# Kernel optimization log

Hardware: AMD Instinct MI355X
Metric: run time of the kernel (lower is better)

## Reference

```python
import jax, jax.numpy as jnp
import numpy as np

NUM_HEADS = 16


def setup_inputs() -> dict:
    key = jax.random.key(0)
    k1, k2, k3 = jax.random.split(key, 3)
    B, S, D = 2, 2048, 1024
    x = jax.random.normal(k1, (B, S, D), dtype=jnp.float32)
    # qkv_bias=False -> no bias on qkv projection; output Dense has default bias
    w_qkv = jax.random.normal(k2, (D, 3 * D), dtype=jnp.float32) * (1.0 / np.sqrt(D))
    w_out = jax.random.normal(k3, (D, D), dtype=jnp.float32) * (1.0 / np.sqrt(D))
    b_out = jnp.zeros((D,), dtype=jnp.float32)
    return {"x": x, "w_qkv": w_qkv, "w_out": w_out, "b_out": b_out}


def reference(x, w_qkv, w_out, b_out):
    B, S, D = x.shape
    H = NUM_HEADS
    Dh = D // H
    scale = 1.0 / np.sqrt(Dh).astype(np.float32)

    qkv = jnp.einsum('bsd,de->bse', x, w_qkv)           # [B,S,3D]
    q, k, v = jnp.split(qkv, 3, axis=-1)
    split = lambda t: t.reshape(B, S, H, Dh).transpose(0, 2, 1, 3)  # [B,H,S,Dh]
    q, k, v = split(q), split(k), split(v)

    attn = jnp.einsum('bhid,bhjd->bhij', q, k) * scale  # [B,H,S,S]
    # mask=None -> all-ones mask combined with causal mask => causal float mask
    causal = jnp.tril(jnp.ones((S, S), dtype=jnp.float32))[None, None]
    attn = causal * attn + (1.0 - causal) * (-1e9)
    attn = jax.nn.softmax(attn, axis=-1)

    out = jnp.einsum('bhij,bhjd->bhid', attn, v)        # [B,H,S,Dh]
    out = out.transpose(0, 2, 1, 3).reshape(B, S, D)    # merge heads
    return jnp.einsum('bsd,de->bse', out, w_out) + b_out
```

## Files before the change

kernel.cpp:

```cpp
#include <hip/hip_runtime.h>

typedef unsigned short u16;
typedef __bf16 bf16x8 __attribute__((ext_vector_type(8)));
typedef unsigned short u16x8 __attribute__((ext_vector_type(8)));
typedef float f32x4 __attribute__((ext_vector_type(4)));

union Frag { u16x8 u; bf16x8 b; };

__device__ __forceinline__ u16 f2bf(float f) {
  unsigned u = __builtin_bit_cast(unsigned, f);
  u += 0x7fff + ((u >> 16) & 1);
  return (u16)(u >> 16);
}

__device__ __forceinline__ f32x4 mfma16(bf16x8 a, bf16x8 b, f32x4 c) {
  return __builtin_amdgcn_mfma_f32_16x16x32_bf16(a, b, c, 0, 0, 0);
}

__device__ __forceinline__ float exp2_raw(float x) {
  float r;
  asm("v_exp_f32 %0, %1" : "=v"(r) : "v"(x));
  return r;
}

typedef const __attribute__((address_space(1))) void* as1cv;
typedef __attribute__((address_space(3))) void* as3v;

__device__ __forceinline__ void glds16(const u16* g, u16* l) {
  __builtin_amdgcn_global_load_lds((as1cv)g, (as3v)l, 16, 0, 0);
}

__global__ __launch_bounds__(256) void prep(const float* __restrict__ x,
                                            u16* __restrict__ xb,
                                            const float* __restrict__ wqkv,
                                            u16* __restrict__ wqkvT,
                                            const float* __restrict__ wout,
                                            u16* __restrict__ woutT) {
  __shared__ float tile[32][33];
  int bid = blockIdx.x;
  int tid = threadIdx.x;
  if (bid >= 4096) {
    int i = (bid - 4096) * 256 + tid;
    const int stride = 1024 * 256;
#pragma unroll
    for (int k = 0; k < 4; ++k) {
      float4 v = ((const float4*)x)[i];
      ushort4 o;
      o.x = f2bf(v.x); o.y = f2bf(v.y); o.z = f2bf(v.z); o.w = f2bf(v.w);
      ((ushort4*)xb)[i] = o;
      i += stride;
    }
    return;
  }
  const float* src; u16* dst; int N;
  if (bid < 3072) { src = wqkv; dst = wqkvT; N = 3072; }
  else            { bid -= 3072; src = wout; dst = woutT; N = 1024; }
  const int K = 1024;
  int tn = N >> 5;
  int bk = bid / tn, bn = bid % tn;
  int k0 = bk << 5, n0 = bn << 5;
  int tx = tid & 31, ty = tid >> 5;
#pragma unroll
  for (int i = 0; i < 4; i++)
    tile[ty + 8 * i][tx] = src[(size_t)(k0 + ty + 8 * i) * N + n0 + tx];
  __syncthreads();
#pragma unroll
  for (int i = 0; i < 4; i++)
    dst[(size_t)(n0 + ty + 8 * i) * K + k0 + tx] = f2bf(tile[tx][ty + 8 * i]);
}

__global__ __launch_bounds__(256) void gemm_qkv(const u16* __restrict__ A,
                                                const u16* __restrict__ BT,
                                                u16* __restrict__ C,
                                                u16* __restrict__ vt,
                                                int N, int K, int nbc) {
  __shared__ u16 Al[2][128 * 32];
  __shared__ u16 Bl[2][128 * 32];
  int nwg = gridDim.x;
  int bid = blockIdx.x;
  int swz = (bid & 7) * (nwg >> 3) + (bid >> 3);
  int br = swz / nbc, bc = swz % nbc;
  int tid = threadIdx.x;
  int w = tid >> 6, l = tid & 63;
  int lg = l >> 4, lq = l & 15;
  int wr = w >> 1, wc = w & 1;

  f32x4 acc[4][4];
#pragma unroll
  for (int m = 0; m < 4; m++)
#pragma unroll
    for (int n = 0; n < 4; n++)
      acc[m][n] = (f32x4){0.f, 0.f, 0.f, 0.f};

  const u16* Ab = A + (size_t)(br * 128 + 32 * w + (l >> 2)) * K + (l & 3) * 8;
  const u16* Bb = BT + (size_t)(bc * 128 + 32 * w + (l >> 2)) * K + (l & 3) * 8;

  auto stage = [&](int it, int buf) {
    int kt = it * 32;
    u16* ald = &Al[buf][32 * w * 32];
    u16* bld = &Bl[buf][32 * w * 32];
    glds16(Ab + kt, ald);
    glds16(Ab + (size_t)16 * K + kt, ald + 16 * 32);
    glds16(Bb + kt, bld);
    glds16(Bb + (size_t)16 * K + kt, bld + 16 * 32);
  };

  int nk = K >> 5;
  stage(0, 0);
  __syncthreads();

  for (int it = 0; it < nk; ++it) {
    int buf = it & 1;
    if (it + 1 < nk) stage(it + 1, buf ^ 1);

    Frag af[4], bf[4];
#pragma unroll
    for (int m = 0; m < 4; m++)
      af[m].u = *(const u16x8*)(&Al[buf][(64 * wr + 16 * m + lq) * 32 + lg * 8]);
#pragma unroll
    for (int n = 0; n < 4; n++)
      bf[n].u = *(const u16x8*)(&Bl[buf][(64 * wc + 16 * n + lq) * 32 + lg * 8]);
    __builtin_amdgcn_s_setprio(1);
#pragma unroll
    for (int m = 0; m < 4; m++)
#pragma unroll
      for (int n = 0; n < 4; n++)
        acc[m][n] = mfma16(af[m].b, bf[n].b, acc[m][n]);
    __builtin_amdgcn_s_setprio(0);
    __syncthreads();
  }

  int row0 = br * 128 + 64 * wr + lg * 4;
  int col0 = bc * 128 + 64 * wc + lq;
  if (bc < 16) {
#pragma unroll
    for (int n = 0; n < 4; n++)
#pragma unroll
      for (int m = 0; m < 4; m++)
#pragma unroll
        for (int r = 0; r < 4; r++)
          C[(size_t)(row0 + 16 * m + r) * N + col0 + 16 * n] = f2bf(acc[m][n][r]);
  } else {
    u16* stbuf = (w == 0) ? &Al[0][0] : (w == 1) ? &Al[1][0]
               : (w == 2) ? &Bl[0][0] : &Bl[1][0];
#pragma unroll
    for (int m = 0; m < 4; m++)
#pragma unroll
      for (int r = 0; r < 4; r++) {
        int srow = 16 * m + 4 * lg + r;
        int X = ((srow >> 2) & 7) << 3;
#pragma unroll
        for (int n = 0; n < 4; n++)
          stbuf[srow * 64 + ((16 * n + lq) ^ X)] = f2bf(acc[m][n][r]);
      }
    int a = l >> 3, bgrp = l & 7;
    int s_base = br * 128 + 64 * wr;
    int bb = s_base >> 11;
    int sblk = (s_base & 2047) >> 6;
    int hh = ((bc - 16) << 1) | wc;
    size_t vbase = ((size_t)(bb * 16 + hh) * 32 + sblk) * 4096;
#pragma unroll
    for (int j = 0; j < 8; ++j) {
      int dh = 8 * j + a;
      u16x8 v;
#pragma unroll
      for (int i = 0; i < 8; ++i) {
        int srow = ((bgrp >> 2) << 5) | (((i >> 2) & 1) << 4) |
                   ((bgrp & 3) << 2) | (i & 3);
        int X = ((srow >> 2) & 7) << 3;
        v[i] = stbuf[srow * 64 + (dh ^ X)];
      }
      *(u16x8*)&vt[vbase + dh * 64 + bgrp * 8] = v;
    }
  }
}

__global__ __launch_bounds__(256) void gemm_bt(const u16* __restrict__ A,
                                               const u16* __restrict__ BT,
                                               float* __restrict__ Cout,
                                               const float* __restrict__ bias,
                                               int N, int K, int nbc) {
  __shared__ u16 Al[2][128 * 32];
  __shared__ u16 Bl[2][128 * 32];
  int nwg = gridDim.x;
  int bid = blockIdx.x;
  int swz = (bid & 7) * (nwg >> 3) + (bid >> 3);
  int br = swz / nbc, bc = swz % nbc;
  int tid = threadIdx.x;
  int w = tid >> 6, l = tid & 63;
  int lg = l >> 4, lq = l & 15;
  int wr = w >> 1, wc = w & 1;

  f32x4 acc[4][4];
#pragma unroll
  for (int m = 0; m < 4; m++)
#pragma unroll
    for (int n = 0; n < 4; n++)
      acc[m][n] = (f32x4){0.f, 0.f, 0.f, 0.f};

  const u16* Ab = A + (size_t)(br * 128 + 32 * w + (l >> 2)) * K + (l & 3) * 8;
  const u16* Bb = BT + (size_t)(bc * 128 + 32 * w + (l >> 2)) * K + (l & 3) * 8;

  auto stage = [&](int it, int buf) {
    int kt = it * 32;
    u16* ald = &Al[buf][32 * w * 32];
    u16* bld = &Bl[buf][32 * w * 32];
    glds16(Ab + kt, ald);
    glds16(Ab + (size_t)16 * K + kt, ald + 16 * 32);
    glds16(Bb + kt, bld);
    glds16(Bb + (size_t)16 * K + kt, bld + 16 * 32);
  };

  int nk = K >> 5;
  stage(0, 0);
  __syncthreads();

  for (int it = 0; it < nk; ++it) {
    int buf = it & 1;
    if (it + 1 < nk) stage(it + 1, buf ^ 1);

    Frag af[4], bf[4];
#pragma unroll
    for (int m = 0; m < 4; m++)
      af[m].u = *(const u16x8*)(&Al[buf][(64 * wr + 16 * m + lq) * 32 + lg * 8]);
#pragma unroll
    for (int n = 0; n < 4; n++)
      bf[n].u = *(const u16x8*)(&Bl[buf][(64 * wc + 16 * n + lq) * 32 + lg * 8]);
    __builtin_amdgcn_s_setprio(1);
#pragma unroll
    for (int m = 0; m < 4; m++)
#pragma unroll
      for (int n = 0; n < 4; n++)
        acc[m][n] = mfma16(af[m].b, bf[n].b, acc[m][n]);
    __builtin_amdgcn_s_setprio(0);
    __syncthreads();
  }

  int row0 = br * 128 + 64 * wr + lg * 4;
  int col0 = bc * 128 + 64 * wc + lq;
#pragma unroll
  for (int n = 0; n < 4; n++) {
    float bv = bias[col0 + 16 * n];
#pragma unroll
    for (int m = 0; m < 4; m++)
#pragma unroll
      for (int r = 0; r < 4; r++)
        Cout[(size_t)(row0 + 16 * m + r) * N + col0 + 16 * n] = acc[m][n][r] + bv;
  }
}

__global__ __launch_bounds__(256) void flash_attn(const u16* __restrict__ qkv,
                                                  const u16* __restrict__ vt,
                                                  u16* __restrict__ aout) {
  __shared__ __align__(16) u16 pool[2][8192];
  const float SL2E = 0.18033688011112043f;
  int bid = blockIdx.x;
  int bh = bid & 31;
  int g = bid >> 5;
  int qb = (g < 8) ? (31 - g) : (g < 16) ? (g - 8) : (g < 24) ? (39 - g) : (g - 16);
  int b = bh >> 4, h = bh & 15;
  int tid = threadIdx.x;
  int w = tid >> 6, l = tid & 63;
  int lg = l >> 4, lq = l & 15;
  int q0w = qb * 64 + w * 16;
  int qidx = q0w + lq;

  const size_t rs = 3072;
  int srw = l >> 3;
  int scol = 8 * ((l & 7) ^ srw);
  const u16* kg = qkv + (size_t)(b * 2048) * rs + 1024 + h * 64;
  const u16* vg = vt + (size_t)bh * 32 * 4096;
  int r0 = (w * 2 + 0) * 8 + srw;
  int r1 = (w * 2 + 1) * 8 + srw;
  int swz = (lq & 7) << 3;

  Frag qf0, qf1;
  const u16* qbase = qkv + (size_t)(b * 2048 + q0w + lq) * rs + h * 64 + lg * 8;
  qf0.u = *(const u16x8*)(qbase);
  qf1.u = *(const u16x8*)(qbase + 32);

  f32x4 lam4 = {0.f, 0.f, 0.f, 0.f};
  f32x4 o[4];
#pragma unroll
  for (int d = 0; d < 4; ++d) o[d] = (f32x4){0.f, 0.f, 0.f, 0.f};

  auto stage = [&](int tile, int buf) {
    int kt2 = tile * 64;
    u16* nb = &pool[buf][0];
    glds16(kg + (size_t)(kt2 + r0) * rs + scol, nb + (w * 2 + 0) * 512);
    glds16(kg + (size_t)(kt2 + r1) * rs + scol, nb + (w * 2 + 1) * 512);
    glds16(vg + (size_t)kt2 * 64 + r0 * 64 + scol, nb + 4096 + (w * 2 + 0) * 512);
    glds16(vg + (size_t)kt2 * 64 + r1 * 64 + scol, nb + 4096 + (w * 2 + 1) * 512);
  };

  stage(0, 0);
  __syncthreads();

  for (int t = 0; t < qb; ++t) {
    stage(t + 1, (t + 1) & 1);
    const u16* Kl = &pool[t & 1][0];
    const u16* Vl = &pool[t & 1][4096];

    f32x4 s[4];
    __builtin_amdgcn_s_setprio(1);
#pragma unroll
    for (int sub = 0; sub < 4; ++sub) {
      int row = sub * 16 + lq;
      Frag k0, k1;
      k0.u = *(const u16x8*)(Kl + row * 64 + ((lg * 8) ^ swz));
      k1.u = *(const u16x8*)(Kl + row * 64 + ((32 + lg * 8) ^ swz));
      f32x4 z = {0.f, 0.f, 0.f, 0.f};
      s[sub] = mfma16(k0.b, qf0.b, z);
      s[sub] = mfma16(k1.b, qf1.b, s[sub]);
    }
    __builtin_amdgcn_s_setprio(0);

    Frag vf[4][2];
#pragma unroll
    for (int d = 0; d < 4; ++d) {
      int row = d * 16 + lq;
      vf[d][0].u = *(const u16x8*)(Vl + row * 64 + ((lg * 8) ^ swz));
      vf[d][1].u = *(const u16x8*)(Vl + row * 64 + ((32 + lg * 8) ^ swz));
    }

    Frag pf[2];
#pragma unroll
    for (int hf = 0; hf < 2; ++hf)
#pragma unroll
      for (int r = 0; r < 4; ++r) {
        float p0 = exp2_raw(s[2 * hf][r] * SL2E);
        float p1 = exp2_raw(s[2 * hf + 1][r] * SL2E);
        lam4[r] += p0 + p1;
        pf[hf].b[r] = (__bf16)p0;
        pf[hf].b[4 + r] = (__bf16)p1;
      }

    __builtin_amdgcn_s_setprio(1);
#pragma unroll
    for (int d = 0; d < 4; ++d) {
      o[d] = mfma16(vf[d][0].b, pf[0].b, o[d]);
      o[d] = mfma16(vf[d][1].b, pf[1].b, o[d]);
    }
    __builtin_amdgcn_s_setprio(0);
    __syncthreads();
  }

  {
    const u16* Kl = &pool[qb & 1][0];
    const u16* Vl = &pool[qb & 1][4096];
    int kt = qb * 64;

    f32x4 s[4];
    __builtin_amdgcn_s_setprio(1);
#pragma unroll
    for (int sub = 0; sub < 4; ++sub) {
      int row = sub * 16 + lq;
      Frag k0, k1;
      k0.u = *(const u16x8*)(Kl + row * 64 + ((lg * 8) ^ swz));
      k1.u = *(const u16x8*)(Kl + row * 64 + ((32 + lg * 8) ^ swz));
      f32x4 z = {0.f, 0.f, 0.f, 0.f};
      s[sub] = mfma16(k0.b, qf0.b, z);
      s[sub] = mfma16(k1.b, qf1.b, s[sub]);
    }
    __builtin_amdgcn_s_setprio(0);

    Frag vf[4][2];
#pragma unroll
    for (int d = 0; d < 4; ++d) {
      int row = d * 16 + lq;
      vf[d][0].u = *(const u16x8*)(Vl + row * 64 + ((lg * 8) ^ swz));
      vf[d][1].u = *(const u16x8*)(Vl + row * 64 + ((32 + lg * 8) ^ swz));
    }

#pragma unroll
    for (int sub = 0; sub < 4; ++sub)
#pragma unroll
      for (int r = 0; r < 4; ++r) {
        int key = kt + sub * 16 + lg * 4 + r;
        if (key > qidx) s[sub][r] = -1e30f;
      }

    Frag pf[2];
#pragma unroll
    for (int hf = 0; hf < 2; ++hf)
#pragma unroll
      for (int r = 0; r < 4; ++r) {
        float p0 = exp2_raw(s[2 * hf][r] * SL2E);
        float p1 = exp2_raw(s[2 * hf + 1][r] * SL2E);
        lam4[r] += p0 + p1;
        pf[hf].b[r] = (__bf16)p0;
        pf[hf].b[4 + r] = (__bf16)p1;
      }

    __builtin_amdgcn_s_setprio(1);
#pragma unroll
    for (int d = 0; d < 4; ++d) {
      o[d] = mfma16(vf[d][0].b, pf[0].b, o[d]);
      o[d] = mfma16(vf[d][1].b, pf[1].b, o[d]);
    }
    __builtin_amdgcn_s_setprio(0);
    __syncthreads();
  }

  float lam = lam4[0] + lam4[1] + lam4[2] + lam4[3];
  lam += __shfl_xor(lam, 16);
  lam += __shfl_xor(lam, 32);
  float inv = 1.0f / lam;

  u16* Ost = &pool[0][0] + w * (16 * 72);
#pragma unroll
  for (int d = 0; d < 4; ++d)
#pragma unroll
    for (int r = 0; r < 4; ++r)
      Ost[lq * 72 + d * 16 + lg * 4 + r] = f2bf(o[d][r] * inv);
  int q = l >> 2, c16 = (l & 3) * 16;
  u16x8 t0, t1;
#pragma unroll
  for (int j = 0; j < 8; j++) { t0[j] = Ost[q * 72 + c16 + j]; t1[j] = Ost[q * 72 + c16 + 8 + j]; }
  u16* orow = aout + (size_t)(b * 2048 + qb * 64 + w * 16 + q) * 1024 + h * 64 + c16;
  *(u16x8*)orow = t0;
  *(u16x8*)(orow + 8) = t1;
}

extern "C" void kernel_launch(void* const* d_in, const int* in_sizes, int n_in,
                              void* d_out, int out_size, void* d_ws, size_t ws_size,
                              hipStream_t stream) {
  const float* x    = (const float*)d_in[0];
  const float* wqkv = (const float*)d_in[1];
  const float* wout = (const float*)d_in[2];
  const float* bout = (const float*)d_in[3];
  float* out = (float*)d_out;

  char* ws = (char*)d_ws;
  u16* xb    = (u16*)(ws);
  u16* wqkvT = (u16*)(ws + 8388608);
  u16* woutT = (u16*)(ws + 14680064);
  u16* qkvb  = (u16*)(ws + 16777216);
  u16* vtb   = (u16*)(ws + 41943040);
  u16* aoutb = (u16*)(ws + 50331648);

  prep<<<5120, 256, 0, stream>>>(x, xb, wqkv, wqkvT, wout, woutT);

  gemm_qkv<<<(4096 / 128) * (3072 / 128), 256, 0, stream>>>(xb, wqkvT, qkvb, vtb,
                                                            3072, 1024, 3072 / 128);
  flash_attn<<<1024, 256, 0, stream>>>(qkvb, vtb, aoutb);

  gemm_bt<<<(4096 / 128) * (1024 / 128), 256, 0, stream>>>(aoutb, woutT, out, bout,
                                                           1024, 1024, 1024 / 128);
}
```

Baseline: 102.2 us.

## Enlarge QKV GEMM tile to 256x256 with 8 waves and triple-buffered LDS

The QKV projection GEMM now uses 256x256 output tiles per workgroup with 512 threads, each wave computing a 128x64 sub-tile. LDS staging moves from double to triple buffering with explicit vmcnt waits and raw barriers, so loads run two stages ahead. This raises operand reuse per LDS byte and hides global latency better. In exchange, register pressure rises (32 accumulators per lane), LDS use grows, and only 192 workgroups are launched, which may underfill the CUs.

```diff
diff --git a/kernel.cpp b/kernel.cpp
--- a/kernel.cpp
+++ b/kernel.cpp
@@ -29,6 +29,8 @@
 __device__ __forceinline__ void glds16(const u16* g, u16* l) {
   __builtin_amdgcn_global_load_lds((as1cv)g, (as3v)l, 16, 0, 0);
 }
+
+#define FENCE asm volatile("" ::: "memory")
 
 __global__ __launch_bounds__(256) void prep(const float* __restrict__ x,
                                             u16* __restrict__ xb,
@@ -69,13 +71,13 @@
     dst[(size_t)(n0 + ty + 8 * i) * K + k0 + tx] = f2bf(tile[tx][ty + 8 * i]);
 }
 
-__global__ __launch_bounds__(256) void gemm_qkv(const u16* __restrict__ A,
+__global__ __launch_bounds__(512) void gemm_qkv(const u16* __restrict__ A,
                                                 const u16* __restrict__ BT,
                                                 u16* __restrict__ C,
                                                 u16* __restrict__ vt,
                                                 int N, int K, int nbc) {
-  __shared__ u16 Al[2][128 * 32];
-  __shared__ u16 Bl[2][128 * 32];
+  __shared__ u16 Al[3][8192];
+  __shared__ u16 Bl[3][8192];
   int nwg = gridDim.x;
   int bid = blockIdx.x;
   int swz = (bid & 7) * (nwg >> 3) + (bid >> 3);
@@ -83,94 +85,103 @@
   int tid = threadIdx.x;
   int w = tid >> 6, l = tid & 63;
   int lg = l >> 4, lq = l & 15;
-  int wr = w >> 1, wc = w & 1;
-
-  f32x4 acc[4][4];
-#pragma unroll
-  for (int m = 0; m < 4; m++)
+  int wr = w >> 2, wc = w & 3;
+
+  f32x4 acc[8][4];
+#pragma unroll
+  for (int m = 0; m < 8; m++)
 #pragma unroll
     for (int n = 0; n < 4; n++)
       acc[m][n] = (f32x4){0.f, 0.f, 0.f, 0.f};
 
-  const u16* Ab = A + (size_t)(br * 128 + 32 * w + (l >> 2)) * K + (l & 3) * 8;
-  const u16* Bb = BT + (size_t)(bc * 128 + 32 * w + (l >> 2)) * K + (l & 3) * 8;
+  const u16* Ab = A + (size_t)(br * 256 + w * 16 + (l >> 2)) * K + (l & 3) * 8;
+  const u16* Bb = BT + (size_t)(bc * 256 + w * 16 + (l >> 2)) * K + (l & 3) * 8;
 
   auto stage = [&](int it, int buf) {
     int kt = it * 32;
-    u16* ald = &Al[buf][32 * w * 32];
-    u16* bld = &Bl[buf][32 * w * 32];
-    glds16(Ab + kt, ald);
-    glds16(Ab + (size_t)16 * K + kt, ald + 16 * 32);
-    glds16(Bb + kt, bld);
-    glds16(Bb + (size_t)16 * K + kt, bld + 16 * 32);
+    glds16(Ab + kt, &Al[buf][w * 512]);
+    glds16(Ab + (size_t)128 * K + kt, &Al[buf][4096 + w * 512]);
+    glds16(Bb + kt, &Bl[buf][w * 512]);
+    glds16(Bb + (size_t)128 * K + kt, &Bl[buf][4096 + w * 512]);
   };
 
   int nk = K >> 5;
   stage(0, 0);
-  __syncthreads();
-
+  stage(1, 1);
+  asm volatile("s_waitcnt vmcnt(4)" ::: "memory");
+  FENCE; __builtin_amdgcn_s_barrier(); FENCE;
+
+  int cur = 0;
   for (int it = 0; it < nk; ++it) {
-    int buf = it & 1;
-    if (it + 1 < nk) stage(it + 1, buf ^ 1);
-
-    Frag af[4], bf[4];
-#pragma unroll
-    for (int m = 0; m < 4; m++)
-      af[m].u = *(const u16x8*)(&Al[buf][(64 * wr + 16 * m + lq) * 32 + lg * 8]);
+    int b2 = cur + 2; if (b2 >= 3) b2 -= 3;
+    if (it + 2 < nk) stage(it + 2, b2);
+
+    Frag a[8], bb[4];
+#pragma unroll
+    for (int m = 0; m < 8; m++)
+      a[m].u = *(const u16x8*)(&Al[cur][(wr * 128 + m * 16 + lq) * 32 + lg * 8]);
 #pragma unroll
     for (int n = 0; n < 4; n++)
-      bf[n].u = *(const u16x8*)(&Bl[buf][(64 * wc + 16 * n + lq) * 32 + lg * 8]);
-    __builtin_amdgcn_s_setprio(1);
-#pragma unroll
-    for (int m = 0; m < 4; m++)
+      bb[n].u = *(const u16x8*)(&Bl[cur][(wc * 64 + n * 16 + lq) * 32 + lg * 8]);
+    __builtin_amdgcn_s_setprio(1);
+#pragma unroll
+    for (int m = 0; m < 8; m++)
 #pragma unroll
       for (int n = 0; n < 4; n++)
-        acc[m][n] = mfma16(af[m].b, bf[n].b, acc[m][n]);
-    __builtin_amdgcn_s_setprio(0);
+        acc[m][n] = mfma16(a[m].b, bb[n].b, acc[m][n]);
+    __builtin_amdgcn_s_setprio(0);
+
+    if (it + 2 < nk)      asm volatile("s_waitcnt vmcnt(4)" ::: "memory");
+    else if (it + 1 < nk) asm volatile("s_waitcnt vmcnt(0)" ::: "memory");
+    if (it + 1 < nk) { FENCE; __builtin_amdgcn_s_barrier(); FENCE; }
+    cur += 1; if (cur >= 3) cur -= 3;
+  }
+
+  int col0 = bc * 256 + wc * 64 + lq;
+  if (bc < 8) {
+#pragma unroll
+    for (int m = 0; m < 8; m++) {
+      int row0 = br * 256 + wr * 128 + m * 16 + lg * 4;
+#pragma unroll
+      for (int n = 0; n < 4; n++)
+#pragma unroll
+        for (int r = 0; r < 4; r++)
+          C[(size_t)(row0 + r) * N + col0 + 16 * n] = f2bf(acc[m][n][r]);
+    }
+  } else {
     __syncthreads();
-  }
-
-  int row0 = br * 128 + 64 * wr + lg * 4;
-  int col0 = bc * 128 + 64 * wc + lq;
-  if (bc < 16) {
-#pragma unroll
-    for (int n = 0; n < 4; n++)
-#pragma unroll
-      for (int m = 0; m < 4; m++)
-#pragma unroll
-        for (int r = 0; r < 4; r++)
-          C[(size_t)(row0 + 16 * m + r) * N + col0 + 16 * n] = f2bf(acc[m][n][r]);
-  } else {
-    u16* stbuf = (w == 0) ? &Al[0][0] : (w == 1) ? &Al[1][0]
-               : (w == 2) ? &Bl[0][0] : &Bl[1][0];
-#pragma unroll
-    for (int m = 0; m < 4; m++)
-#pragma unroll
-      for (int r = 0; r < 4; r++) {
-        int srow = 16 * m + 4 * lg + r;
-        int X = ((srow >> 2) & 7) << 3;
-#pragma unroll
-        for (int n = 0; n < 4; n++)
-          stbuf[srow * 64 + ((16 * n + lq) ^ X)] = f2bf(acc[m][n][r]);
+    u16* stbuf = &Al[0][0] + w * 4096;
+    int hh = (bc - 8) * 4 + wc;
+    int a_ = l >> 3, bgrp = l & 7;
+#pragma unroll
+    for (int sb = 0; sb < 2; ++sb) {
+#pragma unroll
+      for (int mm = 0; mm < 4; mm++)
+#pragma unroll
+        for (int r = 0; r < 4; r++) {
+          int srow = 16 * mm + 4 * lg + r;
+          int X = ((srow >> 2) & 7) << 3;
+#pragma unroll
+          for (int n = 0; n < 4; n++)
+            stbuf[srow * 64 + ((16 * n + lq) ^ X)] = f2bf(acc[sb * 4 + mm][n][r]);
+        }
+      int s_abs = br * 256 + wr * 128 + sb * 64;
+      int bb_ = s_abs >> 11;
+      int sblk = (s_abs & 2047) >> 6;
+      size_t vbase = ((size_t)(bb_ * 16 + hh) * 32 + sblk) * 4096;
+#pragma unroll
+      for (int j = 0; j < 8; ++j) {
+        int dh = 8 * j + a_;
+        u16x8 v;
+#pragma unroll
+        for (int i = 0; i < 8; ++i) {
+          int srow = ((bgrp >> 2) << 5) | (((i >> 2) & 1) << 4) |
+                     ((bgrp & 3) << 2) | (i & 3);
+          int X = ((srow >> 2) & 7) << 3;
+          v[i] = stbuf[srow * 64 + (dh ^ X)];
+        }
+        *(u16x8*)&vt[vbase + dh * 64 + bgrp * 8] = v;
       }
-    int a = l >> 3, bgrp = l & 7;
-    int s_base = br * 128 + 64 * wr;
-    int bb = s_base >> 11;
-    int sblk = (s_base & 2047) >> 6;
-    int hh = ((bc - 16) << 1) | wc;
-    size_t vbase = ((size_t)(bb * 16 + hh) * 32 + sblk) * 4096;
-#pragma unroll
-    for (int j = 0; j < 8; ++j) {
-      int dh = 8 * j + a;
-      u16x8 v;
-#pragma unroll
-      for (int i = 0; i < 8; ++i) {
-        int srow = ((bgrp >> 2) << 5) | (((i >> 2) & 1) << 4) |
-                   ((bgrp & 3) << 2) | (i & 3);
-        int X = ((srow >> 2) & 7) << 3;
-        v[i] = stbuf[srow * 64 + (dh ^ X)];
-      }
-      *(u16x8*)&vt[vbase + dh * 64 + bgrp * 8] = v;
     }
   }
 }
@@ -441,8 +452,8 @@
 
   prep<<<5120, 256, 0, stream>>>(x, xb, wqkv, wqkvT, wout, woutT);
 
-  gemm_qkv<<<(4096 / 128) * (3072 / 128), 256, 0, stream>>>(xb, wqkvT, qkvb, vtb,
-                                                            3072, 1024, 3072 / 128);
+  gemm_qkv<<<(4096 / 256) * (3072 / 256), 512, 0, stream>>>(xb, wqkvT, qkvb, vtb,
+                                                            3072, 1024, 3072 / 256);
   flash_attn<<<1024, 256, 0, stream>>>(qkvb, vtb, aoutb);
 
   gemm_bt<<<(4096 / 128) * (1024 / 128), 256, 0, stream>>>(aoutb, woutT, out, bout,
```

Measured after the change: 111.6 us. 1.09x slower.
